# Optimization experiments

Measured on AMD Instinct MI355X. Metric: run time of the kernel, lower is better.

Reference implementation:

```python
import jax, jax.numpy as jnp
import numpy as np

B, N, D, H = 8, 2048, 128, 8
HD = D // H  # head_depth = 16
CLIP = 10.0
INF = 1e10
THETA = 10000.0
SCALE_BASE = 512.0
LOGIT_SCALE = float(np.log(400.0) / np.log(50.0) / np.sqrt(HD))


def _rotate_half(x):
    # interleaved pairs: (x1, x2) -> (-x2, x1)
    x1 = x[..., ::2]
    x2 = x[..., 1::2]
    return jnp.stack((-x2, x1), axis=-1).reshape(x.shape)


def _rope_xpos(n, hd):
    # rotary_embedding_torch RotaryEmbedding(dim=hd, use_xpos=True)
    inv_freq = 1.0 / (THETA ** (jnp.arange(0, hd, 2, dtype=jnp.float32) / hd))  # (hd/2,)
    t = jnp.arange(n, dtype=jnp.float32)
    freqs = t[:, None] * inv_freq[None, :]          # (n, hd/2)
    freqs = jnp.repeat(freqs, 2, axis=-1)           # (n, hd) interleaved dup
    sc = (jnp.arange(0, hd, 2, dtype=jnp.float32) + 0.4 * hd) / (1.4 * hd)  # (hd/2,)
    power = (t - (n // 2)) / SCALE_BASE             # centered positions
    scale = sc[None, :] ** power[:, None]           # (n, hd/2)
    scale = jnp.repeat(scale, 2, axis=-1)           # (n, hd)
    return freqs, scale


def setup_inputs() -> dict:
    key = jax.random.key(0)
    ks = jax.random.split(key, 7)
    stdv_qkv = 1.0 / np.sqrt(HD)
    stdv_out = 1.0 / np.sqrt(D)
    q = jax.random.normal(ks[0], (B, N, D), dtype=jnp.float32)
    k = jax.random.normal(ks[1], (B, N, D), dtype=jnp.float32)
    v = jax.random.normal(ks[2], (B, N, D), dtype=jnp.float32)
    Wq = jax.random.uniform(ks[3], (D, D), minval=-stdv_qkv, maxval=stdv_qkv, dtype=jnp.float32)
    Wk = jax.random.uniform(ks[4], (D, D), minval=-stdv_qkv, maxval=stdv_qkv, dtype=jnp.float32)
    Wv = jax.random.uniform(ks[5], (D, D), minval=-stdv_qkv, maxval=stdv_qkv, dtype=jnp.float32)
    Wout = jax.random.uniform(ks[6], (D, D), minval=-stdv_out, maxval=stdv_out, dtype=jnp.float32)
    mask = jnp.zeros((B, N, 1), dtype=bool)
    return {"q": q, "k": k, "v": v, "Wq": Wq, "Wk": Wk, "Wv": Wv, "Wout": Wout, "mask": mask}


def reference(q, k, v, Wq, Wk, Wv, Wout, mask):
    def split_heads(t, W):
        # torch Linear (bias=False): t @ W.T, then (B,N,H,HD) -> (B,H,N,HD)
        return (t @ W.T).reshape(B, N, H, HD).transpose(0, 2, 1, 3)

    Qh = split_heads(q, Wq)
    Kh = split_heads(k, Wk)
    Vh = split_heads(v, Wv)

    freqs, scale = _rope_xpos(N, HD)  # (N, HD) each, broadcast over (B,H,N,HD)
    cos, sin = jnp.cos(freqs), jnp.sin(freqs)
    Qr = Qh * (cos * scale) + _rotate_half(Qh) * (sin * scale)
    inv_scale = 1.0 / scale
    Kr = Kh * (cos * inv_scale) + _rotate_half(Kh) * (sin * inv_scale)

    logits = jnp.einsum('bhqd,bhkd->bhqk', Qr, Kr) * LOGIT_SCALE
    logits = CLIP * jnp.tanh(logits)
    # mask: (B,N,1) bool, True -> masked; broadcast to (B,1,1,N)
    logits = jnp.where(mask[:, None, None, :, 0], -INF, logits)
    probs = jax.nn.softmax(logits, axis=-1)
    out = jnp.einsum('bhqk,bhkd->bhqd', probs, Vh)
    out = out.transpose(0, 2, 1, 3).reshape(B, N, D)
    return out @ Wout.T
```

## Files before the change

### kernel.cpp

```cpp
#include <hip/hip_runtime.h>
#include <math.h>

#define BB 8
#define NN 2048
#define DD 128
#define HH 8

typedef _Float16 v4h __attribute__((ext_vector_type(4)));
typedef float    v4f __attribute__((ext_vector_type(4)));

__device__ __forceinline__ v4f zero4() { v4f z = {0.f, 0.f, 0.f, 0.f}; return z; }

__device__ __forceinline__ v4f mfma16(v4h a, v4h b, v4f c) {
    return __builtin_amdgcn_mfma_f32_16x16x16f16(a, b, c, 0, 0, 0);
}

__device__ __forceinline__ float fexp2(float x) {
#if __has_builtin(__builtin_amdgcn_exp2f)
    return __builtin_amdgcn_exp2f(x);
#else
    return __expf(x * 0.69314718055994531f);
#endif
}

#define QSCALE 1.10478088f
#define C1F 14.426950408889634f
#define C2F 28.853900817779268f

__global__ __launch_bounds__(256) void prep_kernel(
    const float* __restrict__ Wq, const float* __restrict__ Wk,
    const float* __restrict__ Wv, const float* __restrict__ Wo,
    _Float16* __restrict__ WH, _Float16* __restrict__ WoH,
    float* __restrict__ rtab)
{
    int tid = blockIdx.x * 256 + threadIdx.x;
    int m = tid >> 14, i = tid & 16383;
    const float* src = (m == 0) ? Wq : (m == 1) ? Wk : (m == 2) ? Wv : Wo;
    float wv = src[i];
    if (m < 3) WH[m * 16384 + i] = (_Float16)wv;
    else       WoH[i] = (_Float16)wv;

    if (tid < NN * 16) {
        int t = tid >> 4, hd = tid & 15, j = hd >> 1;
        const float invf_tab[8] = {1.f, 0.31622776601683794f, 0.1f, 0.031622776601683791f,
                                   0.01f, 0.0031622776601683794f, 0.001f, 0.00031622776601683794f};
        float freq = (float)t * invf_tab[j];
        float c = cosf(freq), s = sinf(freq);
        float scf = ((float)(2 * j) + 6.4f) / 22.4f;
        float pw  = ((float)t - 1024.0f) / 512.0f;
        float scl = exp2f(pw * log2f(scf));
        rtab[0 * NN * 16 + tid] = c * scl * QSCALE;
        rtab[1 * NN * 16 + tid] = s * scl * QSCALE;
        float is = 1.0f / scl;
        rtab[2 * NN * 16 + tid] = c * is;
        rtab[3 * NN * 16 + tid] = s * is;
    }
}

__global__ __launch_bounds__(256) void proj_rope_kernel(
    const float* __restrict__ q, const float* __restrict__ k, const float* __restrict__ v,
    const _Float16* __restrict__ WH, const float* __restrict__ rtab,
    _Float16* __restrict__ Qr, _Float16* __restrict__ Kr, _Float16* __restrict__ VT)
{
    __shared__ __align__(16) _Float16 xb[64][136];
    const int tid = threadIdx.x;
    const int m  = blockIdx.y;
    const int r0 = blockIdx.x * 64;
    const int b  = r0 >> 11;
    const int n0 = r0 & 2047;

    const float* s = ((m == 0) ? q : (m == 1) ? k : v) + (size_t)r0 * 128;
    #pragma unroll
    for (int i = 0; i < 8; ++i) {
        int u = tid + i * 256;
        int row = u >> 5, c4 = (u & 31) * 4;
        v4f f = *(const v4f*)(s + row * 128 + c4);
        v4h hv; hv[0]=(_Float16)f[0]; hv[1]=(_Float16)f[1]; hv[2]=(_Float16)f[2]; hv[3]=(_Float16)f[3];
        *(v4h*)&xb[row][c4] = hv;
    }
    __syncthreads();

    const int w = tid >> 6, lane = tid & 63;
    const int l16 = lane & 15, quad = lane >> 4;

    v4h xf[8];
    #pragma unroll
    for (int kt = 0; kt < 8; ++kt)
        xf[kt] = *(const v4h*)&xb[w * 16 + l16][kt * 16 + quad * 4];
    const _Float16* Wm = WH + m * 16384;
    v4f acc[8];
    #pragma unroll
    for (int ct = 0; ct < 8; ++ct) acc[ct] = zero4();
    #pragma unroll
    for (int kt = 0; kt < 8; ++kt) {
        #pragma unroll
        for (int ct = 0; ct < 8; ++ct) {
            v4h wf = *(const v4h*)(Wm + (ct * 16 + l16) * 128 + kt * 16 + quad * 4);
            if (m < 2) acc[ct] = mfma16(wf, xf[kt], acc[ct]);
            else       acc[ct] = mfma16(xf[kt], wf, acc[ct]);
        }
    }
    if (m < 2) {
        const float* tc = rtab + (m == 0 ? 0 : 2 * NN * 16);
        const float* ts = tc + NN * 16;
        const int n = n0 + w * 16 + l16;
        _Float16* dst = (m == 0 ? Qr : Kr);
        #pragma unroll
        for (int ct = 0; ct < 8; ++ct) {
            v4f cs = *(const v4f*)(tc + n * 16 + quad * 4);
            v4f sn = *(const v4f*)(ts + n * 16 + quad * 4);
            v4f a = acc[ct];
            v4f rot; rot[0] = -a[1]; rot[1] = a[0]; rot[2] = -a[3]; rot[3] = a[2];
            v4h o;
            #pragma unroll
            for (int r = 0; r < 4; ++r) o[r] = (_Float16)(a[r] * cs[r] + rot[r] * sn[r]);
            *(v4h*)(dst + ((size_t)(b * 8 + ct) * NN + n) * 16 + quad * 4) = o;
        }
    } else {
        #pragma unroll
        for (int ct = 0; ct < 8; ++ct) {
            v4f a = acc[ct];
            v4h o;
            #pragma unroll
            for (int r = 0; r < 4; ++r) o[r] = (_Float16)a[r];
            *(v4h*)(VT + ((size_t)(b * 8 + ct) * 16 + l16) * NN + n0 + w * 16 + quad * 4) = o;
        }
    }
}

__global__ __launch_bounds__(256) void attn_kernel(
    const _Float16* __restrict__ Qr, const _Float16* __restrict__ Kr,
    const _Float16* __restrict__ VT, const unsigned char* __restrict__ mask,
    _Float16* __restrict__ Obuf)
{
    __shared__ __align__(16) _Float16 Kt[64][20];
    __shared__ __align__(16) _Float16 VTt[16][72];
    __shared__ __align__(16) float    av[64];

    const int tid = threadIdx.x;
    const int bh = blockIdx.x >> 4;
    const int qt = blockIdx.x & 15;
    const int b = bh >> 3, h = bh & 7;
    const int q0 = qt * 128;
    const int w = tid >> 6, lane = tid & 63;
    const int l16 = lane & 15, quad = lane >> 4;

    v4h qf[2];
    #pragma unroll
    for (int g = 0; g < 2; ++g) {
        int qrow = q0 + w * 32 + g * 16 + l16;
        qf[g] = *(const v4h*)(Qr + ((size_t)bh * NN + qrow) * 16 + quad * 4);
    }
    v4f ot[2]; ot[0] = zero4(); ot[1] = zero4();
    v4f sa[2]; sa[0] = zero4(); sa[1] = zero4();
    v4h ones; ones[0] = ones[1] = ones[2] = ones[3] = (_Float16)1.f;

    const int srow = tid >> 2, sc4 = (tid & 3) * 4;
    const int vhd = tid >> 4, vn4 = (tid & 15) * 4;

    for (int k0 = 0; k0 < NN; k0 += 64) {
        __syncthreads();
        *(v4h*)&Kt[srow][sc4]  = *(const v4h*)(Kr + ((size_t)bh * NN + k0 + srow) * 16 + sc4);
        *(v4h*)&VTt[vhd][vn4]  = *(const v4h*)(VT + ((size_t)bh * 16 + vhd) * NN + k0 + vn4);
        if (tid < 64) av[tid] = mask[b * NN + k0 + tid] ? -1e30f : C1F;
        __syncthreads();

        #pragma unroll
        for (int st = 0; st < 4; ++st) {
            v4h kf = *(const v4h*)&Kt[st * 16 + l16][quad * 4];
            v4f ad = *(const v4f*)&av[st * 16 + quad * 4];
            v4h vf = *(const v4h*)&VTt[l16][st * 16 + quad * 4];
            #pragma unroll
            for (int g = 0; g < 2; ++g) {
                v4f sv = mfma16(kf, qf[g], zero4());
                v4h ph;
                #pragma unroll
                for (int r = 0; r < 4; ++r) {
                    float u  = fexp2(sv[r]);
                    float rc = __builtin_amdgcn_rcpf(u + 1.f);
                    float p  = fexp2(__builtin_fmaf(rc, -C2F, ad[r]));
                    ph[r] = (_Float16)p;
                }
                ot[g] = mfma16(vf, ph, ot[g]);
                sa[g] = mfma16(ones, ph, sa[g]);
            }
        }
    }
    #pragma unroll
    for (int g = 0; g < 2; ++g) {
        float rd = 1.0f / sa[g][0];
        v4h o;
        #pragma unroll
        for (int r = 0; r < 4; ++r) o[r] = (_Float16)(ot[g][r] * rd);
        int qrow = q0 + w * 32 + g * 16 + l16;
        *(v4h*)(Obuf + ((size_t)(b * NN + qrow) * 128) + h * 16 + quad * 4) = o;
    }
}

__global__ __launch_bounds__(256) void outproj_kernel(
    const _Float16* __restrict__ Obuf, const _Float16* __restrict__ WoH,
    float* __restrict__ out)
{
    __shared__ __align__(16) _Float16 ob[64][136];
    const int tid = threadIdx.x;
    const int r0 = blockIdx.x * 64;
    const int ct0 = blockIdx.y * 4;
    #pragma unroll
    for (int i = 0; i < 8; ++i) {
        int u = tid + i * 256;
        int row = u >> 5, c4 = (u & 31) * 4;
        *(v4h*)&ob[row][c4] = *(const v4h*)(Obuf + (size_t)(r0 + row) * 128 + c4);
    }
    __syncthreads();
    const int w = tid >> 6, lane = tid & 63;
    const int l16 = lane & 15, quad = lane >> 4;
    v4h af[8];
    #pragma unroll
    for (int kt = 0; kt < 8; ++kt)
        af[kt] = *(const v4h*)&ob[w * 16 + l16][kt * 16 + quad * 4];
    v4f acc[4];
    #pragma unroll
    for (int c = 0; c < 4; ++c) acc[c] = zero4();
    #pragma unroll
    for (int kt = 0; kt < 8; ++kt)
        #pragma unroll
        for (int c = 0; c < 4; ++c) {
            v4h wf = *(const v4h*)(WoH + ((ct0 + c) * 16 + l16) * 128 + kt * 16 + quad * 4);
            acc[c] = mfma16(af[kt], wf, acc[c]);
        }
    #pragma unroll
    for (int c = 0; c < 4; ++c)
        #pragma unroll
        for (int r = 0; r < 4; ++r)
            out[(size_t)(r0 + w * 16 + quad * 4 + r) * 128 + (ct0 + c) * 16 + l16] = acc[c][r];
}

extern "C" void kernel_launch(void* const* d_in, const int* in_sizes, int n_in,
                              void* d_out, int out_size, void* d_ws, size_t ws_size,
                              hipStream_t stream)
{
    const float* q  = (const float*)d_in[0];
    const float* k  = (const float*)d_in[1];
    const float* v  = (const float*)d_in[2];
    const float* Wq = (const float*)d_in[3];
    const float* Wk = (const float*)d_in[4];
    const float* Wv = (const float*)d_in[5];
    const float* Wo = (const float*)d_in[6];
    const unsigned char* mask = (const unsigned char*)d_in[7];
    float* out = (float*)d_out;

    char* ws = (char*)d_ws;
    _Float16* WH   = (_Float16*)(ws);
    _Float16* WoH  = (_Float16*)(ws + 98304);
    float*    rtab = (float*)(ws + 131072);
    _Float16* Qr   = (_Float16*)(ws + 655360);
    _Float16* Kr   = (_Float16*)(ws + 4849664);
    _Float16* VTd  = (_Float16*)(ws + 9043968);
    _Float16* Obuf = (_Float16*)(ws + 13238272);

    prep_kernel<<<256, 256, 0, stream>>>(Wq, Wk, Wv, Wo, WH, WoH, rtab);
    proj_rope_kernel<<<dim3(256, 3), 256, 0, stream>>>(q, k, v, WH, rtab, Qr, Kr, VTd);
    attn_kernel<<<1024, 256, 0, stream>>>(Qr, Kr, VTd, mask, Obuf);
    outproj_kernel<<<dim3(256, 2), 256, 0, stream>>>(Obuf, WoH, out);
}
```

Baseline: 211.1 us.

## Use single-wave attention blocks with register-prefetched double-buffered K/V tiles

The attention kernel now launches 64-thread blocks, each a single wavefront covering 64 queries (four 16-row groups), instead of 256-thread blocks of four waves covering 32 queries each. The next K/V/mask tile is loaded into registers before the current tile's MFMA and exp work, then written into the other half of a double-buffered LDS area. Because each block is one wave, both __syncthreads barriers are gone. The aim is to hide global-load latency, drop barrier stalls, and reuse each K/V tile across more queries. In exchange, register pressure rises and the grid has half as many waves, so there is less wave-level parallelism per CU.

New measurement: 212.2 us. No clear change (+0.6%).

```diff
diff --git a/kernel.cpp b/kernel.cpp
--- a/kernel.cpp
+++ b/kernel.cpp
@@ -8,6 +8,7 @@
 
 typedef _Float16 v4h __attribute__((ext_vector_type(4)));
 typedef float    v4f __attribute__((ext_vector_type(4)));
+struct h8 { v4h a, b; };
 
 __device__ __forceinline__ v4f zero4() { v4f z = {0.f, 0.f, 0.f, 0.f}; return z; }
 
@@ -128,72 +129,95 @@
     }
 }
 
-__global__ __launch_bounds__(256) void attn_kernel(
+__global__ __launch_bounds__(64) void attn_kernel(
     const _Float16* __restrict__ Qr, const _Float16* __restrict__ Kr,
     const _Float16* __restrict__ VT, const unsigned char* __restrict__ mask,
     _Float16* __restrict__ Obuf)
 {
-    __shared__ __align__(16) _Float16 Kt[64][20];
-    __shared__ __align__(16) _Float16 VTt[16][72];
-    __shared__ __align__(16) float    av[64];
+    __shared__ __align__(16) _Float16 Kt[2][64][20];
+    __shared__ __align__(16) _Float16 VTt[2][16][68];
+    __shared__ __align__(16) float    av[2][64];
 
     const int tid = threadIdx.x;
-    const int bh = blockIdx.x >> 4;
-    const int qt = blockIdx.x & 15;
+    const int bh = blockIdx.x >> 5;
+    const int qt = blockIdx.x & 31;
     const int b = bh >> 3, h = bh & 7;
-    const int q0 = qt * 128;
-    const int w = tid >> 6, lane = tid & 63;
-    const int l16 = lane & 15, quad = lane >> 4;
-
-    v4h qf[2];
-    #pragma unroll
-    for (int g = 0; g < 2; ++g) {
-        int qrow = q0 + w * 32 + g * 16 + l16;
-        qf[g] = *(const v4h*)(Qr + ((size_t)bh * NN + qrow) * 16 + quad * 4);
-    }
-    v4f ot[2]; ot[0] = zero4(); ot[1] = zero4();
-    v4f sa[2]; sa[0] = zero4(); sa[1] = zero4();
+    const int q0 = qt * 64;
+    const int l16 = tid & 15, quad = tid >> 4;
+
+    const _Float16* Kbase = Kr + (size_t)bh * NN * 16;
+    const _Float16* Vbase = VT + (size_t)bh * 16 * NN;
+    const unsigned char* mbase = mask + b * NN;
+
+    v4h qf[4];
+    #pragma unroll
+    for (int g = 0; g < 4; ++g)
+        qf[g] = *(const v4h*)(Qr + ((size_t)bh * NN + q0 + g * 16 + l16) * 16 + quad * 4);
+
+    v4f ot[4], sa[4];
+    #pragma unroll
+    for (int g = 0; g < 4; ++g) { ot[g] = zero4(); sa[g] = zero4(); }
     v4h ones; ones[0] = ones[1] = ones[2] = ones[3] = (_Float16)1.f;
 
-    const int srow = tid >> 2, sc4 = (tid & 3) * 4;
-    const int vhd = tid >> 4, vn4 = (tid & 15) * 4;
-
-    for (int k0 = 0; k0 < NN; k0 += 64) {
-        __syncthreads();
-        *(v4h*)&Kt[srow][sc4]  = *(const v4h*)(Kr + ((size_t)bh * NN + k0 + srow) * 16 + sc4);
-        *(v4h*)&VTt[vhd][vn4]  = *(const v4h*)(VT + ((size_t)bh * 16 + vhd) * NN + k0 + vn4);
-        if (tid < 64) av[tid] = mask[b * NN + k0 + tid] ? -1e30f : C1F;
-        __syncthreads();
+    const int vrow = tid >> 2, vcol = (tid & 3) * 16;
+
+    {
+        h8 kA = *(const h8*)(Kbase + (size_t)tid * 16);
+        h8 kB = *(const h8*)(Kbase + (size_t)tid * 16 + 8);
+        h8 vA = *(const h8*)(Vbase + (size_t)vrow * NN + vcol);
+        h8 vB = *(const h8*)(Vbase + (size_t)vrow * NN + vcol + 8);
+        float a0 = mbase[tid] ? -1e30f : C1F;
+        *(v4h*)&Kt[0][tid][0]  = kA.a;  *(v4h*)&Kt[0][tid][4]  = kA.b;
+        *(v4h*)&Kt[0][tid][8]  = kB.a;  *(v4h*)&Kt[0][tid][12] = kB.b;
+        *(v4h*)&VTt[0][vrow][vcol]      = vA.a;  *(v4h*)&VTt[0][vrow][vcol + 4]  = vA.b;
+        *(v4h*)&VTt[0][vrow][vcol + 8]  = vB.a;  *(v4h*)&VTt[0][vrow][vcol + 12] = vB.b;
+        av[0][tid] = a0;
+    }
+
+    for (int t = 0; t < 32; ++t) {
+        const int cur = t & 1, nxt = cur ^ 1;
+        const int nk = ((t + 1) & 31) * 64;
+
+        h8 kA = *(const h8*)(Kbase + (size_t)(nk + tid) * 16);
+        h8 kB = *(const h8*)(Kbase + (size_t)(nk + tid) * 16 + 8);
+        h8 vA = *(const h8*)(Vbase + (size_t)vrow * NN + nk + vcol);
+        h8 vB = *(const h8*)(Vbase + (size_t)vrow * NN + nk + vcol + 8);
+        float an = mbase[nk + tid] ? -1e30f : C1F;
 
         #pragma unroll
         for (int st = 0; st < 4; ++st) {
-            v4h kf = *(const v4h*)&Kt[st * 16 + l16][quad * 4];
-            v4f ad = *(const v4f*)&av[st * 16 + quad * 4];
-            v4h vf = *(const v4h*)&VTt[l16][st * 16 + quad * 4];
+            v4h kf = *(const v4h*)&Kt[cur][st * 16 + l16][quad * 4];
+            v4f ad = *(const v4f*)&av[cur][st * 16 + quad * 4];
+            v4h vf = *(const v4h*)&VTt[cur][l16][st * 16 + quad * 4];
             #pragma unroll
-            for (int g = 0; g < 2; ++g) {
+            for (int g = 0; g < 4; ++g) {
                 v4f sv = mfma16(kf, qf[g], zero4());
                 v4h ph;
                 #pragma unroll
                 for (int r = 0; r < 4; ++r) {
                     float u  = fexp2(sv[r]);
                     float rc = __builtin_amdgcn_rcpf(u + 1.f);
-                    float p  = fexp2(__builtin_fmaf(rc, -C2F, ad[r]));
-                    ph[r] = (_Float16)p;
+                    ph[r] = (_Float16)fexp2(__builtin_fmaf(rc, -C2F, ad[r]));
                 }
                 ot[g] = mfma16(vf, ph, ot[g]);
                 sa[g] = mfma16(ones, ph, sa[g]);
             }
         }
-    }
-    #pragma unroll
-    for (int g = 0; g < 2; ++g) {
+
+        *(v4h*)&Kt[nxt][tid][0]  = kA.a;  *(v4h*)&Kt[nxt][tid][4]  = kA.b;
+        *(v4h*)&Kt[nxt][tid][8]  = kB.a;  *(v4h*)&Kt[nxt][tid][12] = kB.b;
+        *(v4h*)&VTt[nxt][vrow][vcol]      = vA.a;  *(v4h*)&VTt[nxt][vrow][vcol + 4]  = vA.b;
+        *(v4h*)&VTt[nxt][vrow][vcol + 8]  = vB.a;  *(v4h*)&VTt[nxt][vrow][vcol + 12] = vB.b;
+        av[nxt][tid] = an;
+    }
+
+    #pragma unroll
+    for (int g = 0; g < 4; ++g) {
         float rd = 1.0f / sa[g][0];
         v4h o;
         #pragma unroll
         for (int r = 0; r < 4; ++r) o[r] = (_Float16)(ot[g][r] * rd);
-        int qrow = q0 + w * 32 + g * 16 + l16;
-        *(v4h*)(Obuf + ((size_t)(b * NN + qrow) * 128) + h * 16 + quad * 4) = o;
+        *(v4h*)(Obuf + ((size_t)(b * NN + q0 + g * 16 + l16) * 128) + h * 16 + quad * 4) = o;
     }
 }
 
@@ -260,6 +284,6 @@
 
     prep_kernel<<<256, 256, 0, stream>>>(Wq, Wk, Wv, Wo, WH, WoH, rtab);
     proj_rope_kernel<<<dim3(256, 3), 256, 0, stream>>>(q, k, v, WH, rtab, Qr, Kr, VTd);
-    attn_kernel<<<1024, 256, 0, stream>>>(Qr, Kr, VTd, mask, Obuf);
+    attn_kernel<<<2048, 64, 0, stream>>>(Qr, Kr, VTd, mask, Obuf);
     outproj_kernel<<<dim3(256, 2), 256, 0, stream>>>(Obuf, WoH, out);
 }
```
